# Kernel tuning notes

Hardware: AMD Instinct MI355X
Metric: run time of the kernel (lower is better)

Reference implementation:

```python
import jax, jax.numpy as jnp
import numpy as np

K = 3          # kernel size
S = 1          # stride
P = 1          # padding
D = 1          # dilation
KK = K * K


def conv2d(x, w, b):
    # plain conv for the offset branch, NCHW/OIHW
    out = jax.lax.conv_general_dilated(
        x, w, window_strides=(S, S), padding=[(P, P), (P, P)],
        rhs_dilation=(D, D), dimension_numbers=('NCHW', 'OIHW', 'NCHW'))
    return out + b[None, :, None, None]


def deform_conv2d(x, offset, w, b):
    # torchvision-style deformable conv (groups=1, no modulation mask)
    B, C, H, W = x.shape
    Cout = w.shape[0]
    Ho, Wo = offset.shape[2], offset.shape[3]
    # offset channels are interleaved (dy, dx) per kernel tap
    off = offset.reshape(B, KK, 2, Ho, Wo)
    dy, dx = off[:, :, 0], off[:, :, 1]                      # [B,KK,Ho,Wo]

    ki, kj = jnp.meshgrid(jnp.arange(K), jnp.arange(K), indexing='ij')
    ki = ki.reshape(KK).astype(x.dtype)
    kj = kj.reshape(KK).astype(x.dtype)
    base_y = (jnp.arange(Ho) * S - P).astype(x.dtype)
    base_x = (jnp.arange(Wo) * S - P).astype(x.dtype)
    # absolute sampling coords per (b, tap, ho, wo)
    py = base_y[None, None, :, None] + (ki * D)[None, :, None, None] + dy
    px = base_x[None, None, None, :] + (kj * D)[None, :, None, None] + dx

    y0f = jnp.floor(py)
    x0f = jnp.floor(px)
    wy1 = py - y0f
    wx1 = px - x0f
    wy0 = 1.0 - wy1
    wx0 = 1.0 - wx1
    y0 = y0f.astype(jnp.int32)
    x0 = x0f.astype(jnp.int32)

    x_flat = x.reshape(B, C, H * W)

    def gather(yi, xi):
        # zero-padded gather at integer corner (yi, xi): [B,KK,Ho,Wo] -> [B,C,KK,Ho,Wo]
        valid = (yi >= 0) & (yi < H) & (xi >= 0) & (xi < W)
        idx = jnp.clip(yi, 0, H - 1) * W + jnp.clip(xi, 0, W - 1)
        v = jax.vmap(lambda xf, i: xf[:, i])(x_flat, idx.reshape(B, -1))
        v = v.reshape(B, C, KK, Ho, Wo)
        return v * valid[:, None].astype(x.dtype)

    v00 = gather(y0, x0)
    v01 = gather(y0, x0 + 1)
    v10 = gather(y0 + 1, x0)
    v11 = gather(y0 + 1, x0 + 1)

    sampled = ((wy0 * wx0)[:, None] * v00 + (wy0 * wx1)[:, None] * v01 +
               (wy1 * wx0)[:, None] * v10 + (wy1 * wx1)[:, None] * v11)
    # implicit GEMM over (Cin, kernel taps)
    out = jnp.einsum('bckhw,ock->bohw', sampled, w.reshape(Cout, C, KK))
    return out + b[None, :, None, None]


def setup_inputs() -> dict:
    key = jax.random.key(0)
    k1, k2, k3 = jax.random.split(key, 3)
    B, Cin, Cout, H, W = 32, 64, 64, 64, 64
    x = jax.random.normal(k1, (B, Cin, H, W), dtype=jnp.float32)
    # small but nonzero offset weights so bilinear sampling is exercised
    w_offset = jax.random.normal(k2, (2 * KK, Cin, K, K), dtype=jnp.float32) * 0.01
    b_offset = jnp.zeros((2 * KK,), dtype=jnp.float32)
    fan_in = Cin * KK
    w_conv = jax.random.normal(k3, (Cout, Cin, K, K), dtype=jnp.float32) * (1.0 / np.sqrt(fan_in))
    b_conv = jnp.zeros((Cout,), dtype=jnp.float32)
    return {'x': x, 'w_offset': w_offset, 'b_offset': b_offset,
            'w_conv': w_conv, 'b_conv': b_conv}


def reference(x, w_offset, b_offset, w_conv, b_conv):
    offset = conv2d(x, w_offset, b_offset)       # [B, 2*K*K, Ho, Wo]
    return deform_conv2d(x, offset, w_conv, b_conv)
```

## Files before the change

### kernel.cpp

```cpp
#include <hip/hip_runtime.h>
#include <hip/hip_bf16.h>

#define CIN  64
#define COUT 64
#define HH   64
#define WW   64
#define HW   4096
#define OFFC 18
#define KK2  9
#define II   576
#define NP   16
#define SMPW (II + 8)
#define NKC  (II / 32)
#define IMGB (HW * CIN * 2)

typedef __attribute__((ext_vector_type(8))) short  short8;
typedef __attribute__((ext_vector_type(4))) float  f32x4;

__device__ __forceinline__ float u2f(unsigned int u) {
    union { unsigned int i; float f; } v; v.i = u; return v.f;
}
__device__ __forceinline__ short8 as_short8(uint4 u) {
    union { uint4 a; short8 b; } v; v.a = u; return v.b;
}
__device__ __forceinline__ unsigned short f2bf_bits(float f) {
    union { __hip_bfloat16 b; unsigned short s; } cv;
    cv.b = __float2bfloat16(f);
    return cv.s;
}

__global__ __launch_bounds__(256) void prep(const float* __restrict__ x,
                                            const float* __restrict__ wc,
                                            const float* __restrict__ w,
                                            __hip_bfloat16* __restrict__ xT,
                                            __hip_bfloat16* __restrict__ wmp,
                                            __hip_bfloat16* __restrict__ bop) {
    const int t = threadIdx.x;
    if (blockIdx.x < 2048) {
        __shared__ float tile[64][68];
        const int b = blockIdx.x >> 6, h = blockIdx.x & 63;
        {
            const int w4 = t & 15, cg = t >> 4;
            #pragma unroll
            for (int i = 0; i < 4; ++i) {
                const int c = cg + i * 16;
                const float4 v = *(const float4*)&x[((b * 64 + c) * 64 + h) * 64 + w4 * 4];
                *(float4*)&tile[c][w4 * 4] = v;
            }
        }
        __syncthreads();
        {
            const int ww = t & 63, c0 = (t >> 6) * 16;
            unsigned int pk[8];
            #pragma unroll
            for (int ci = 0; ci < 8; ++ci) {
                const unsigned int lo = f2bf_bits(tile[c0 + 2 * ci][ww]);
                const unsigned int hi = f2bf_bits(tile[c0 + 2 * ci + 1][ww]);
                pk[ci] = lo | (hi << 16);
            }
            char* dst = (char*)xT + (size_t)(((b * 64 + h) * 64 + ww) * 64 + c0) * 2;
            uint4 v0, v1;
            v0.x = pk[0]; v0.y = pk[1]; v0.z = pk[2]; v0.w = pk[3];
            v1.x = pk[4]; v1.y = pk[5]; v1.z = pk[6]; v1.w = pk[7];
            *(uint4*)dst = v0;
            *(uint4*)(dst + 16) = v1;
        }
    } else {
        const int idx = (blockIdx.x - 2048) * 256 + t;
        if (idx < 4 * NKC * 64 * 8) {
            const int j    = idx & 7;
            const int lane = (idx >> 3) & 63;
            const int kc   = (idx >> 9) % NKC;
            const int nt   = idx / (NKC * 512);
            const int o  = nt * 16 + (lane & 15);
            const int ks = kc * 32 + (lane >> 4) * 8 + j;
            const int c  = ks & 63, kk = ks >> 6;
            wmp[idx] = __float2bfloat16(wc[(o * CIN + c) * KK2 + kk]);
        } else {
            const int i2 = idx - 4 * NKC * 64 * 8;
            const int j    = i2 & 7;
            const int lane = (i2 >> 3) & 63;
            const int kc   = (i2 >> 9) % NKC;
            const int nt   = i2 / (NKC * 512);
            const int ch = nt * 16 + (lane & 15);
            const int ks = kc * 32 + (lane >> 4) * 8 + j;
            const int c  = ks & 63, kk = ks >> 6;
            bop[i2] = (ch < OFFC) ? __float2bfloat16(w[(ch * CIN + c) * KK2 + kk])
                                  : __float2bfloat16(0.f);
        }
    }
}

__global__ __launch_bounds__(256, 6) void deform_fused(const __hip_bfloat16* __restrict__ xT,
                                                       const __hip_bfloat16* __restrict__ bop,
                                                       const __hip_bfloat16* __restrict__ wmp,
                                                       const float* __restrict__ boff,
                                                       const float* __restrict__ bconv,
                                                       float* __restrict__ out) {
    __shared__ __hip_bfloat16 smp[NP][SMPW];
    __shared__ uint4 metal[NP * KK2];

    const int t = threadIdx.x;
    const int wave = t >> 6, lane = t & 63;
    const int sp0g = blockIdx.x * NP;
    const int b = sp0g >> 12, sp0 = sp0g & 4095;
    const int ho = sp0 >> 6, wo0 = sp0 & 63;
    const char* xbB = (const char*)xT + (size_t)b * IMGB;

    f32x4 acc0 = {0.f, 0.f, 0.f, 0.f};
    f32x4 acc1 = {0.f, 0.f, 0.f, 0.f};
    {
        const int m = lane & 15, quad = lane >> 4;
        const short8* bp = (const short8*)bop;
        for (int kk = wave; kk < KK2; kk += 4) {
            const int ki = kk / 3, kj = kk - ki * 3;
            const int y = ho - 1 + ki;
            if ((unsigned)y < HH) {
                const int col = wo0 + m + kj - 1;
                const int ccl = min(max(col, 0), WW - 1);
                const bool ok = (unsigned)col < WW;
                const char* base = xbB + (y * 64 + ccl) * 128 + quad * 16;
                uint4 v0 = *(const uint4*)(base);
                uint4 v1 = *(const uint4*)(base + 64);
                if (!ok) { v0.x = v0.y = v0.z = v0.w = 0u; v1.x = v1.y = v1.z = v1.w = 0u; }
                const int kc0 = 2 * kk, kc1 = 2 * kk + 1;
                acc0 = __builtin_amdgcn_mfma_f32_16x16x32_bf16(as_short8(v0), bp[kc0 * 64 + lane], acc0, 0, 0, 0);
                acc1 = __builtin_amdgcn_mfma_f32_16x16x32_bf16(as_short8(v0), bp[(NKC + kc0) * 64 + lane], acc1, 0, 0, 0);
                acc0 = __builtin_amdgcn_mfma_f32_16x16x32_bf16(as_short8(v1), bp[kc1 * 64 + lane], acc0, 0, 0, 0);
                acc1 = __builtin_amdgcn_mfma_f32_16x16x32_bf16(as_short8(v1), bp[(NKC + kc1) * 64 + lane], acc1, 0, 0, 0);
            }
        }
        float* pacc = (float*)&smp[0][0];
        const int n = lane & 15;
        #pragma unroll
        for (int r = 0; r < 4; ++r) {
            const int p = quad * 4 + r;
            pacc[(wave * 16 + p) * 20 + n] = acc0[r];
            if (n < 2) pacc[(wave * 16 + p) * 20 + 16 + n] = acc1[r];
        }
    }
    __syncthreads();

    {
        float* pacc = (float*)&smp[0][0];
        float* offs = pacc + 4 * 16 * 20;
        for (int e = t; e < NP * OFFC; e += 256) {
            const int p = e / OFFC, ch = e - p * OFFC;
            offs[p * 20 + ch] = boff[ch]
                + pacc[p * 20 + ch] + pacc[(16 + p) * 20 + ch]
                + pacc[(32 + p) * 20 + ch] + pacc[(48 + p) * 20 + ch];
        }
    }
    __syncthreads();

    if (t < NP * KK2) {
        const float* offs = (const float*)&smp[0][0] + 4 * 16 * 20;
        const int p = t / KK2, kk = t - p * KK2;
        const int wo = wo0 + p;
        const float dy = offs[p * 20 + 2 * kk];
        const float dx = offs[p * 20 + 2 * kk + 1];
        const int ki = kk / 3, kj = kk - ki * 3;
        const float py = (float)(ho - 1 + ki) + dy;
        const float px = (float)(wo - 1 + kj) + dx;
        const float y0f = floorf(py), x0f = floorf(px);
        const int y0 = (int)y0f, x0 = (int)x0f;
        const float wy1 = py - y0f, wx1 = px - x0f;
        const float wy0 = 1.f - wy1, wx0 = 1.f - wx1;
        const int yb = min(max(y0, 0), HH - 2);
        const int zb = min(max(x0, 0), WW - 2);
        const float vy0 = ((unsigned)y0 < HH) ? wy0 : 0.f;
        const float vy1 = ((unsigned)(y0 + 1) < HH) ? wy1 : 0.f;
        const float vx0 = ((unsigned)x0 < WW) ? wx0 : 0.f;
        const float vx1 = ((unsigned)(x0 + 1) < WW) ? wx1 : 0.f;
        const float t0 = (y0 == yb ? vy0 : 0.f) + (y0 + 1 == yb ? vy1 : 0.f);
        const float t1 = (y0 == yb + 1 ? vy0 : 0.f) + (y0 + 1 == yb + 1 ? vy1 : 0.f);
        const float u0 = (x0 == zb ? vx0 : 0.f) + (x0 + 1 == zb ? vx1 : 0.f);
        const float u1 = (x0 == zb + 1 ? vx0 : 0.f) + (x0 + 1 == zb + 1 ? vx1 : 0.f);
        union { unsigned int u; _Float16 h[2]; } c0, c1;
        c0.h[0] = (_Float16)(t0 * u0); c0.h[1] = (_Float16)(t1 * u0);
        c1.h[0] = (_Float16)(t0 * u1); c1.h[1] = (_Float16)(t1 * u1);
        uint4 mt;
        mt.x = (unsigned int)((yb * 64 + zb) * 128);
        mt.y = c0.u; mt.z = c1.u; mt.w = 0u;
        metal[t] = mt;
    }
    __syncthreads();

    {
        const int li = lane & 31;
        const int h  = lane >> 5;
        const char* xli = xbB + li * 4;
        for (int q = 0; q < 4; ++q) {
            const int p = wave * 4 + q;
            uint4 mtj[5];
            #pragma unroll
            for (int j = 0; j < 5; ++j) {
                const int kk = min(2 * j + h, 8);
                mtj[j] = metal[p * KK2 + kk];
            }
            unsigned int rg[5][4];
            #pragma unroll
            for (int j = 0; j < 5; ++j) {
                const char* base = xli + (int)mtj[j].x;
                rg[j][0] = *(const unsigned int*)(base);
                rg[j][1] = *(const unsigned int*)(base + 128);
                rg[j][2] = *(const unsigned int*)(base + 8192);
                rg[j][3] = *(const unsigned int*)(base + 8320);
            }
            #pragma unroll
            for (int j = 0; j < 5; ++j) {
                union { unsigned int u; _Float16 f[2]; } c0, c1;
                c0.u = mtj[j].y; c1.u = mtj[j].z;
                const float w00 = (float)c0.f[0], w10 = (float)c0.f[1];
                const float w01 = (float)c1.f[0], w11 = (float)c1.f[1];
                const float a0l = u2f(rg[j][0] << 16), a0h = u2f(rg[j][0] & 0xffff0000u);
                const float a1l = u2f(rg[j][1] << 16), a1h = u2f(rg[j][1] & 0xffff0000u);
                const float b0l = u2f(rg[j][2] << 16), b0h = u2f(rg[j][2] & 0xffff0000u);
                const float b1l = u2f(rg[j][3] << 16), b1h = u2f(rg[j][3] & 0xffff0000u);
                const float vl = w00 * a0l + w01 * a1l + w10 * b0l + w11 * b1l;
                const float vh = w00 * a0h + w01 * a1h + w10 * b0h + w11 * b1h;
                const int kk = min(2 * j + h, 8);
                __hip_bfloat162 pk;
                pk.x = __float2bfloat16(vl);
                pk.y = __float2bfloat16(vh);
                *(__hip_bfloat162*)((char*)&smp[p][0] + kk * 128 + li * 4) = pk;
            }
        }
    }
    __syncthreads();

    f32x4 acc = {0.f, 0.f, 0.f, 0.f};
    {
        const char* abase = (const char*)&smp[lane & 15][0] + (lane >> 4) * 16;
        const short8* wp = (const short8*)wmp + wave * NKC * 64 + lane;
        #pragma unroll
        for (int kc = 0; kc < NKC; ++kc) {
            const short8 a  = *(const short8*)(abase + kc * 64);
            const short8 bw = wp[kc * 64];
            acc = __builtin_amdgcn_mfma_f32_16x16x32_bf16(a, bw, acc, 0, 0, 0);
        }
    }
    __syncthreads();

    {
        float* outb = (float*)&smp[0][0];
        const int o = wave * 16 + (lane & 15);
        const float bias = bconv[o];
        const int pr = (lane >> 4) * 4;
        #pragma unroll
        for (int r = 0; r < 4; ++r)
            outb[o * 17 + pr + r] = acc[r] + bias;
    }
    __syncthreads();
    {
        const float* outb = (const float*)&smp[0][0];
        const int oo = t >> 2, pxb = (t & 3) * 4;
        const float* lb = outb + oo * 17 + pxb;
        float4 v;
        v.x = lb[0]; v.y = lb[1]; v.z = lb[2]; v.w = lb[3];
        *(float4*)(out + ((size_t)(b * COUT + oo)) * HW + sp0 + pxb) = v;
    }
}

extern "C" void kernel_launch(void* const* d_in, const int* in_sizes, int n_in,
                              void* d_out, int out_size, void* d_ws, size_t ws_size,
                              hipStream_t stream) {
    const float* x      = (const float*)d_in[0];
    const float* w_off  = (const float*)d_in[1];
    const float* b_off  = (const float*)d_in[2];
    const float* w_conv = (const float*)d_in[3];
    const float* b_conv = (const float*)d_in[4];
    float* out = (float*)d_out;

    __hip_bfloat16* xT  = (__hip_bfloat16*)d_ws;
    __hip_bfloat16* wmp = xT + (size_t)32 * HW * CIN;
    __hip_bfloat16* bop = wmp + 4 * NKC * 64 * 8;

    hipLaunchKernelGGL(prep, dim3(2048 + 216), dim3(256), 0, stream,
                       x, w_conv, w_off, xT, wmp, bop);
    hipLaunchKernelGGL(deform_fused, dim3(32 * HW / NP), dim3(256), 0, stream,
                       xT, bop, wmp, b_off, b_conv, out);
}
```

Before: 159.4 us.

## Rebalance offset-conv waves, drop offset-reduce pass, and widen bilinear gather per lane

The offset-conv MFMA loop now spreads the 18 half-tap units across the 4 waves instead of 9 taps, which evens out per-wave work. The separate reduction pass and its barrier are folded into the metadata stage, which sums the per-wave partials directly. The bilinear sampling stage switches to 16 lanes of 8-byte loads covering 36 (pixel, tap) items with no wasted slots, replacing 32 lanes of 4-byte loads that had duplicate clamped taps. Launch bounds are raised to 7 blocks per CU, which tightens the register budget.

```diff
diff --git a/kernel.cpp b/kernel.cpp
--- a/kernel.cpp
+++ b/kernel.cpp
@@ -27,6 +27,9 @@
     union { __hip_bfloat16 b; unsigned short s; } cv;
     cv.b = __float2bfloat16(f);
     return cv.s;
+}
+__device__ __forceinline__ float2 bfpair(unsigned int u) {
+    float2 r; r.x = u2f(u << 16); r.y = u2f(u & 0xffff0000u); return r;
 }
 
 __global__ __launch_bounds__(256) void prep(const float* __restrict__ x,
@@ -91,7 +94,7 @@
     }
 }
 
-__global__ __launch_bounds__(256, 6) void deform_fused(const __hip_bfloat16* __restrict__ xT,
+__global__ __launch_bounds__(256, 7) void deform_fused(const __hip_bfloat16* __restrict__ xT,
                                                        const __hip_bfloat16* __restrict__ bop,
                                                        const __hip_bfloat16* __restrict__ wmp,
                                                        const float* __restrict__ boff,
@@ -112,22 +115,19 @@
     {
         const int m = lane & 15, quad = lane >> 4;
         const short8* bp = (const short8*)bop;
-        for (int kk = wave; kk < KK2; kk += 4) {
+        for (int u = wave; u < 2 * KK2; u += 4) {
+            const int kk = u >> 1, h = u & 1;
             const int ki = kk / 3, kj = kk - ki * 3;
             const int y = ho - 1 + ki;
             if ((unsigned)y < HH) {
                 const int col = wo0 + m + kj - 1;
                 const int ccl = min(max(col, 0), WW - 1);
                 const bool ok = (unsigned)col < WW;
-                const char* base = xbB + (y * 64 + ccl) * 128 + quad * 16;
-                uint4 v0 = *(const uint4*)(base);
-                uint4 v1 = *(const uint4*)(base + 64);
-                if (!ok) { v0.x = v0.y = v0.z = v0.w = 0u; v1.x = v1.y = v1.z = v1.w = 0u; }
-                const int kc0 = 2 * kk, kc1 = 2 * kk + 1;
-                acc0 = __builtin_amdgcn_mfma_f32_16x16x32_bf16(as_short8(v0), bp[kc0 * 64 + lane], acc0, 0, 0, 0);
-                acc1 = __builtin_amdgcn_mfma_f32_16x16x32_bf16(as_short8(v0), bp[(NKC + kc0) * 64 + lane], acc1, 0, 0, 0);
-                acc0 = __builtin_amdgcn_mfma_f32_16x16x32_bf16(as_short8(v1), bp[kc1 * 64 + lane], acc0, 0, 0, 0);
-                acc1 = __builtin_amdgcn_mfma_f32_16x16x32_bf16(as_short8(v1), bp[(NKC + kc1) * 64 + lane], acc1, 0, 0, 0);
+                uint4 v = *(const uint4*)(xbB + (y * 64 + ccl) * 128 + quad * 16 + h * 64);
+                if (!ok) { v.x = 0u; v.y = 0u; v.z = 0u; v.w = 0u; }
+                const int kc = 2 * kk + h;
+                acc0 = __builtin_amdgcn_mfma_f32_16x16x32_bf16(as_short8(v), bp[kc * 64 + lane], acc0, 0, 0, 0);
+                acc1 = __builtin_amdgcn_mfma_f32_16x16x32_bf16(as_short8(v), bp[(NKC + kc) * 64 + lane], acc1, 0, 0, 0);
             }
         }
         float* pacc = (float*)&smp[0][0];
@@ -141,24 +141,18 @@
     }
     __syncthreads();
 
-    {
-        float* pacc = (float*)&smp[0][0];
-        float* offs = pacc + 4 * 16 * 20;
-        for (int e = t; e < NP * OFFC; e += 256) {
-            const int p = e / OFFC, ch = e - p * OFFC;
-            offs[p * 20 + ch] = boff[ch]
-                + pacc[p * 20 + ch] + pacc[(16 + p) * 20 + ch]
-                + pacc[(32 + p) * 20 + ch] + pacc[(48 + p) * 20 + ch];
-        }
-    }
-    __syncthreads();
-
     if (t < NP * KK2) {
-        const float* offs = (const float*)&smp[0][0] + 4 * 16 * 20;
+        const float* pacc = (const float*)&smp[0][0];
         const int p = t / KK2, kk = t - p * KK2;
+        const float2 bb = *(const float2*)&boff[2 * kk];
+        float2 d = bb;
+        #pragma unroll
+        for (int wv = 0; wv < 4; ++wv) {
+            const float2 pp = *(const float2*)&pacc[(wv * 16 + p) * 20 + 2 * kk];
+            d.x += pp.x; d.y += pp.y;
+        }
+        const float dy = d.x, dx = d.y;
         const int wo = wo0 + p;
-        const float dy = offs[p * 20 + 2 * kk];
-        const float dx = offs[p * 20 + 2 * kk + 1];
         const int ki = kk / 3, kj = kk - ki * 3;
         const float py = (float)(ho - 1 + ki) + dy;
         const float px = (float)(wo - 1 + kj) + dx;
@@ -187,44 +181,42 @@
     __syncthreads();
 
     {
-        const int li = lane & 31;
-        const int h  = lane >> 5;
-        const char* xli = xbB + li * 4;
-        for (int q = 0; q < 4; ++q) {
-            const int p = wave * 4 + q;
-            uint4 mtj[5];
-            #pragma unroll
-            for (int j = 0; j < 5; ++j) {
-                const int kk = min(2 * j + h, 8);
-                mtj[j] = metal[p * KK2 + kk];
-            }
-            unsigned int rg[5][4];
-            #pragma unroll
-            for (int j = 0; j < 5; ++j) {
-                const char* base = xli + (int)mtj[j].x;
-                rg[j][0] = *(const unsigned int*)(base);
-                rg[j][1] = *(const unsigned int*)(base + 128);
-                rg[j][2] = *(const unsigned int*)(base + 8192);
-                rg[j][3] = *(const unsigned int*)(base + 8320);
-            }
-            #pragma unroll
-            for (int j = 0; j < 5; ++j) {
-                union { unsigned int u; _Float16 f[2]; } c0, c1;
-                c0.u = mtj[j].y; c1.u = mtj[j].z;
-                const float w00 = (float)c0.f[0], w10 = (float)c0.f[1];
-                const float w01 = (float)c1.f[0], w11 = (float)c1.f[1];
-                const float a0l = u2f(rg[j][0] << 16), a0h = u2f(rg[j][0] & 0xffff0000u);
-                const float a1l = u2f(rg[j][1] << 16), a1h = u2f(rg[j][1] & 0xffff0000u);
-                const float b0l = u2f(rg[j][2] << 16), b0h = u2f(rg[j][2] & 0xffff0000u);
-                const float b1l = u2f(rg[j][3] << 16), b1h = u2f(rg[j][3] & 0xffff0000u);
-                const float vl = w00 * a0l + w01 * a1l + w10 * b0l + w11 * b1l;
-                const float vh = w00 * a0h + w01 * a1h + w10 * b0h + w11 * b1h;
-                const int kk = min(2 * j + h, 8);
-                __hip_bfloat162 pk;
-                pk.x = __float2bfloat16(vl);
-                pk.y = __float2bfloat16(vh);
-                *(__hip_bfloat162*)((char*)&smp[p][0] + kk * 128 + li * 4) = pk;
-            }
+        const int li4 = lane & 15;
+        const int tg  = lane >> 4;
+        const char* xli = xbB + li4 * 8;
+        const int p0 = wave * 4;
+        #pragma unroll
+        for (int s = 0; s < 9; ++s) {
+            const int e  = s * 4 + tg;
+            const int pl = e / 9;
+            const int kk = e - pl * 9;
+            const uint4 mt = metal[p0 * KK2 + e];
+            const char* base = xli + (int)mt.x;
+            const uint2 r00 = *(const uint2*)(base);
+            const uint2 r01 = *(const uint2*)(base + 128);
+            const uint2 r10 = *(const uint2*)(base + 8192);
+            const uint2 r11 = *(const uint2*)(base + 8320);
+            union { unsigned int u; _Float16 h[2]; } c0, c1;
+            c0.u = mt.y; c1.u = mt.z;
+            const float w00 = (float)c0.h[0], w10 = (float)c0.h[1];
+            const float w01 = (float)c1.h[0], w11 = (float)c1.h[1];
+            float2 v0, v1;
+            {
+                const float2 a00 = bfpair(r00.x), a01 = bfpair(r01.x);
+                const float2 a10 = bfpair(r10.x), a11 = bfpair(r11.x);
+                v0.x = w00 * a00.x + w01 * a01.x + w10 * a10.x + w11 * a11.x;
+                v0.y = w00 * a00.y + w01 * a01.y + w10 * a10.y + w11 * a11.y;
+            }
+            {
+                const float2 a00 = bfpair(r00.y), a01 = bfpair(r01.y);
+                const float2 a10 = bfpair(r10.y), a11 = bfpair(r11.y);
+                v1.x = w00 * a00.x + w01 * a01.x + w10 * a10.x + w11 * a11.x;
+                v1.y = w00 * a00.y + w01 * a01.y + w10 * a10.y + w11 * a11.y;
+            }
+            union { struct { __hip_bfloat162 a, b; } s2; uint2 u; } st;
+            st.s2.a = __float22bfloat162_rn(v0);
+            st.s2.b = __float22bfloat162_rn(v1);
+            *(uint2*)((char*)&smp[p0 + pl][0] + kk * 128 + li4 * 8) = st.u;
         }
     }
     __syncthreads();
```

Measured after the change: 170.7 us. 1.07x slower.

## Rebalance offset-conv work across waves, fold offset reduction, unroll sampling loop

Applied to the files above, without the earlier changes.

The offset-conv MFMA loop now splits each kernel tap into two half-channel units, distributing 18 units over 4 waves instead of 9 taps, which evens out per-wave load. The separate reduction pass and its barrier are removed; the threads that compute bilinear metadata sum the four wave partials and the bias directly. Launch bounds are raised to 7 blocks per CU and the sampling loop over q is fully unrolled. Together these aim to cut idle wave time and one sync in the prologue. The higher occupancy target may force register spills, especially with the added unroll.

```diff
diff --git a/kernel.cpp b/kernel.cpp
--- a/kernel.cpp
+++ b/kernel.cpp
@@ -91,7 +91,7 @@
     }
 }
 
-__global__ __launch_bounds__(256, 6) void deform_fused(const __hip_bfloat16* __restrict__ xT,
+__global__ __launch_bounds__(256, 7) void deform_fused(const __hip_bfloat16* __restrict__ xT,
                                                        const __hip_bfloat16* __restrict__ bop,
                                                        const __hip_bfloat16* __restrict__ wmp,
                                                        const float* __restrict__ boff,
@@ -112,22 +112,19 @@
     {
         const int m = lane & 15, quad = lane >> 4;
         const short8* bp = (const short8*)bop;
-        for (int kk = wave; kk < KK2; kk += 4) {
+        for (int u = wave; u < 2 * KK2; u += 4) {
+            const int kk = u >> 1, h = u & 1;
             const int ki = kk / 3, kj = kk - ki * 3;
             const int y = ho - 1 + ki;
             if ((unsigned)y < HH) {
                 const int col = wo0 + m + kj - 1;
                 const int ccl = min(max(col, 0), WW - 1);
                 const bool ok = (unsigned)col < WW;
-                const char* base = xbB + (y * 64 + ccl) * 128 + quad * 16;
-                uint4 v0 = *(const uint4*)(base);
-                uint4 v1 = *(const uint4*)(base + 64);
-                if (!ok) { v0.x = v0.y = v0.z = v0.w = 0u; v1.x = v1.y = v1.z = v1.w = 0u; }
-                const int kc0 = 2 * kk, kc1 = 2 * kk + 1;
-                acc0 = __builtin_amdgcn_mfma_f32_16x16x32_bf16(as_short8(v0), bp[kc0 * 64 + lane], acc0, 0, 0, 0);
-                acc1 = __builtin_amdgcn_mfma_f32_16x16x32_bf16(as_short8(v0), bp[(NKC + kc0) * 64 + lane], acc1, 0, 0, 0);
-                acc0 = __builtin_amdgcn_mfma_f32_16x16x32_bf16(as_short8(v1), bp[kc1 * 64 + lane], acc0, 0, 0, 0);
-                acc1 = __builtin_amdgcn_mfma_f32_16x16x32_bf16(as_short8(v1), bp[(NKC + kc1) * 64 + lane], acc1, 0, 0, 0);
+                uint4 v = *(const uint4*)(xbB + (y * 64 + ccl) * 128 + quad * 16 + h * 64);
+                if (!ok) { v.x = 0u; v.y = 0u; v.z = 0u; v.w = 0u; }
+                const int kc = 2 * kk + h;
+                acc0 = __builtin_amdgcn_mfma_f32_16x16x32_bf16(as_short8(v), bp[kc * 64 + lane], acc0, 0, 0, 0);
+                acc1 = __builtin_amdgcn_mfma_f32_16x16x32_bf16(as_short8(v), bp[(NKC + kc) * 64 + lane], acc1, 0, 0, 0);
             }
         }
         float* pacc = (float*)&smp[0][0];
@@ -141,24 +138,18 @@
     }
     __syncthreads();
 
-    {
-        float* pacc = (float*)&smp[0][0];
-        float* offs = pacc + 4 * 16 * 20;
-        for (int e = t; e < NP * OFFC; e += 256) {
-            const int p = e / OFFC, ch = e - p * OFFC;
-            offs[p * 20 + ch] = boff[ch]
-                + pacc[p * 20 + ch] + pacc[(16 + p) * 20 + ch]
-                + pacc[(32 + p) * 20 + ch] + pacc[(48 + p) * 20 + ch];
-        }
-    }
-    __syncthreads();
-
     if (t < NP * KK2) {
-        const float* offs = (const float*)&smp[0][0] + 4 * 16 * 20;
+        const float* pacc = (const float*)&smp[0][0];
         const int p = t / KK2, kk = t - p * KK2;
+        const float2 bb = *(const float2*)&boff[2 * kk];
+        float2 d = bb;
+        #pragma unroll
+        for (int wv = 0; wv < 4; ++wv) {
+            const float2 pp = *(const float2*)&pacc[(wv * 16 + p) * 20 + 2 * kk];
+            d.x += pp.x; d.y += pp.y;
+        }
+        const float dy = d.x, dx = d.y;
         const int wo = wo0 + p;
-        const float dy = offs[p * 20 + 2 * kk];
-        const float dx = offs[p * 20 + 2 * kk + 1];
         const int ki = kk / 3, kj = kk - ki * 3;
         const float py = (float)(ho - 1 + ki) + dy;
         const float px = (float)(wo - 1 + kj) + dx;
@@ -190,6 +181,7 @@
         const int li = lane & 31;
         const int h  = lane >> 5;
         const char* xli = xbB + li * 4;
+        #pragma unroll
         for (int q = 0; q < 4; ++q) {
             const int p = wave * 4 + q;
             uint4 mtj[5];
```

After: 159.1 us. Within noise of the previous version (-0.2%).
